# Optimization experiments

Measured on AMD Instinct MI355X. Metric: run time of the kernel, lower is better.

## Reference

```python
import jax, jax.numpy as jnp
import numpy as np

B, OBS, H, A, E = 131072, 194, 64, 5, 3  # batch, obs dim, hidden, max_action_dim, n event types


def setup_inputs() -> dict:
    key = jax.random.key(0)
    ks = jax.random.split(key, 16)
    s = lambda k, shape, std=0.1: (jax.random.normal(k, shape, dtype=jnp.float32) * std)
    return {
        "x": jax.random.normal(ks[0], (B, OBS), dtype=jnp.float32),
        "action": jax.random.randint(ks[1], (B,), 0, A),
        "W1": s(ks[2], (OBS, H)), "b1": jnp.zeros((H,), jnp.float32),
        "W2": s(ks[3], (H, H)),   "b2": jnp.zeros((H,), jnp.float32),
        "Wh": s(ks[4], (E, H, A), 0.01), "bh": jnp.zeros((E, A), jnp.float32),
        "Wc1": s(ks[5], (OBS, H)), "bc1": jnp.zeros((H,), jnp.float32),
        "Wc2": s(ks[6], (H, H)),   "bc2": jnp.zeros((H,), jnp.float32),
        "Wc3": s(ks[7], (H, 1)),   "bc3": jnp.zeros((1,), jnp.float32),
    }


def reference(x, action, W1, b1, W2, b2, Wh, bh, Wc1, bc1, Wc2, bc2, Wc3, bc3):
    # shared trunk
    feat = jnp.tanh(jnp.tanh(x @ W1 + b1) @ W2 + b2)          # [B, H]
    # route each sample to one of E heads via argmax of first 3 obs dims
    ev = jnp.argmax(x[:, :E], axis=1)                          # [B] int
    all_logits = jnp.einsum('bh,eha->bea', feat, Wh) + bh      # [B, E, A]
    logits = jnp.take_along_axis(
        all_logits, jnp.broadcast_to(ev[:, None, None], (x.shape[0], 1, A)), axis=1
    )[:, 0]                                                    # [B, A]
    logp_all = jax.nn.log_softmax(logits, axis=-1)             # [B, A]
    logp = jnp.take_along_axis(logp_all, action[:, None], axis=1)[:, 0]  # [B]
    entropy = -jnp.sum(jnp.exp(logp_all) * logp_all, axis=-1)  # [B]
    # critic
    value = jnp.tanh(jnp.tanh(x @ Wc1 + bc1) @ Wc2 + bc2) @ Wc3 + bc3    # [B, 1]
    return action, logp, entropy, value
```

## Files before the change

### kernel.cpp

```cpp
#include <hip/hip_runtime.h>
#include <hip/hip_bf16.h>

constexpr int Bt  = 131072;
constexpr int OBS = 194;
constexpr int NT  = 256;
constexpr int MT  = 64;
constexpr int RS  = 72;
constexpr int LS  = 18;

constexpr int W1B_S  = 0;
constexpr int WC1B_S = 14336;
constexpr int W2B_S  = 28672;
constexpr int WC2B_S = 36864;
constexpr int WHB_S  = 45056;

typedef short bf8   __attribute__((ext_vector_type(8)));
typedef float f32x4 __attribute__((ext_vector_type(4)));
typedef unsigned int u32;

__device__ __forceinline__ short f2bs(float f) {
    union { __hip_bfloat16 h; short s; } u;
    u.h = __float2bfloat16(f);
    return u.s;
}
__device__ __forceinline__ float bs2f(short s) {
    union { short s; __hip_bfloat16 h; } u;
    u.s = s;
    return __bfloat162float(u.h);
}
__device__ __forceinline__ u32 pk2(float a, float b) {
    union { __hip_bfloat162 h; u32 u; } r;
    r.h = __float22bfloat162_rn(float2{a, b});
    return r.u;
}
__device__ __forceinline__ float fast_tanh(float v) {
    v = fminf(fmaxf(v, -15.f), 15.f);
    float e = __expf(2.f * v);
    return (e - 1.f) * __builtin_amdgcn_rcpf(e + 1.f);
}
__device__ __forceinline__ void dma16(const void* g, void* s) {
    __builtin_amdgcn_global_load_lds(
        (const __attribute__((address_space(1))) u32*)g,
        (__attribute__((address_space(3))) u32*)s, 16, 0, 0);
}

__global__ void __launch_bounds__(256) prep(
    const float* __restrict__ W1, const float* __restrict__ b1,
    const float* __restrict__ W2, const float* __restrict__ Wh,
    const float* __restrict__ Wc1, const float* __restrict__ bc1,
    const float* __restrict__ Wc2, const float* __restrict__ Wc3,
    short* __restrict__ ws)
{
    const int gid = blockIdx.x * 256 + threadIdx.x;
    const int gsz = gridDim.x * 256;

    for (int i = gid; i < 14336; i += gsz) {
        int j = i & 7, l = (i >> 3) & 63, nt = (i >> 9) & 3, kb = i >> 11;
        int k = kb * 32 + ((l >> 4) << 3) + j;
        int n = nt * 16 + (l & 15);
        short v1 = 0, v2 = 0;
        if (k < OBS) {
            v1 = f2bs(W1[k * 64 + n]);
            v2 = f2bs(Wc1[k * 64 + n]);
        } else if (k == OBS) {
            v1 = f2bs(b1[n]);
            v2 = f2bs(bc1[n]);
        }
        ws[W1B_S + i]  = v1;
        ws[WC1B_S + i] = v2;
    }
    for (int i = gid; i < 8192; i += gsz) {
        int j = i & 7, l = (i >> 3) & 63, nt = (i >> 9) & 3, kb = i >> 11;
        int s = kb * 32 + ((l >> 4) << 3) + j;
        int kp = (s & 3) * 16 + (s >> 2);
        int n = nt * 16 + (l & 15);
        ws[W2B_S + i]  = f2bs(W2[kp * 64 + n]);
        ws[WC2B_S + i] = f2bs(Wc2[kp * 64 + n]);
    }
    for (int i = gid; i < 1024; i += gsz) {
        int j = i & 7, l = (i >> 3) & 63, kb = i >> 9;
        int s = kb * 32 + ((l >> 4) << 3) + j;
        int kp = (s & 3) * 16 + (s >> 2);
        int cc = l & 15;
        float v;
        if (cc == 15) v = Wc3[kp];
        else { int e = cc / 5, a = cc - 5 * e; v = Wh[(e * 64 + kp) * 5 + a]; }
        ws[WHB_S + i] = f2bs(v);
    }
}

__global__ void __launch_bounds__(NT, 2) fused_ac(
    const float* __restrict__ x, const int* __restrict__ act_in,
    const float* __restrict__ b2, const float* __restrict__ bc2,
    const float* __restrict__ bh, const float* __restrict__ bc3,
    const short* __restrict__ ws,
    float* __restrict__ out)
{
    __shared__ __align__(16) char smem[57344];

    const int t  = threadIdx.x;
    const int w  = t >> 6;
    const int l  = t & 63;
    const int q  = l >> 4;
    const int c  = l & 15;
    const int gm = blockIdx.x * MT + w * 16 + c;

    {
        const char* g = ((const char*)ws) + (size_t)(w * 14) * 1024 + l * 16;
        char* s = smem + (w * 14) * 1024 + l * 16;
        #pragma unroll
        for (int i = 0; i < 14; ++i)
            dma16(g + i * 1024, s + i * 1024);
    }

    float b2v[4], bc2v[4];
    #pragma unroll
    for (int nt = 0; nt < 4; ++nt) {
        b2v[nt]  = b2[nt * 16 + c];
        bc2v[nt] = bc2[nt * 16 + c];
    }
    float bhv = (c < 15) ? bh[c] : bc3[0];
    int act = 0;
    if (l < 16) act = act_in[gm];

    union AF { u32 u[4]; bf8 v; } af[7];
    int ev = 0;
    {
        const float* xr = x + (size_t)gm * OBS;
        #pragma unroll
        for (int kb = 0; kb < 6; ++kb) {
            const float2* p = reinterpret_cast<const float2*>(xr + kb * 32 + q * 8);
            float2 v0 = p[0], v1 = p[1], v2 = p[2], v3 = p[3];
            if (kb == 0 && q == 0) {
                float best = v0.x;
                if (v0.y > best) { best = v0.y; ev = 1; }
                if (v1.x > best) { ev = 2; }
            }
            af[kb].u[0] = pk2(v0.x, v0.y); af[kb].u[1] = pk2(v1.x, v1.y);
            af[kb].u[2] = pk2(v2.x, v2.y); af[kb].u[3] = pk2(v3.x, v3.y);
        }
        af[6].u[0] = 0; af[6].u[1] = 0; af[6].u[2] = 0; af[6].u[3] = 0;
        if (q == 0) {
            float2 v = *reinterpret_cast<const float2*>(xr + 192);
            af[6].u[0] = pk2(v.x, v.y);
            af[6].u[1] = pk2(1.0f, 0.0f);
        }
    }

    __syncthreads();

    const bf8* fW1L  = reinterpret_cast<const bf8*>(smem);
    const bf8* fWc1L = reinterpret_cast<const bf8*>(smem + 28672);
    f32x4 aa[4], ac[4];
    #pragma unroll
    for (int nt = 0; nt < 4; ++nt) {
        aa[nt] = f32x4{0.f, 0.f, 0.f, 0.f};
        ac[nt] = f32x4{0.f, 0.f, 0.f, 0.f};
    }
    #pragma unroll
    for (int kb = 0; kb < 7; ++kb) {
        bf8 a = af[kb].v;
        #pragma unroll
        for (int nt = 0; nt < 4; ++nt) {
            aa[nt] = __builtin_amdgcn_mfma_f32_16x16x32_bf16(a, fW1L [(kb * 4 + nt) * 64 + l], aa[nt], 0, 0, 0);
            ac[nt] = __builtin_amdgcn_mfma_f32_16x16x32_bf16(a, fWc1L[(kb * 4 + nt) * 64 + l], ac[nt], 0, 0, 0);
        }
    }
    #pragma unroll
    for (int nt = 0; nt < 4; ++nt)
        #pragma unroll
        for (int r = 0; r < 4; ++r) {
            aa[nt][r] = fast_tanh(aa[nt][r]);
            ac[nt][r] = fast_tanh(ac[nt][r]);
        }

    __syncthreads();

    {
        const char* g = ((const char*)ws) + 57344 + (size_t)(w * 9) * 1024 + l * 16;
        char* s = smem + (w * 9) * 1024 + l * 16;
        #pragma unroll
        for (int i = 0; i < 9; ++i)
            if (w * 9 + i < 34)
                dma16(g + i * 1024, s + i * 1024);
    }
    short* ha = reinterpret_cast<short*>(smem + 34816 + w * 2304);
    short* hc = reinterpret_cast<short*>(smem + 44032 + w * 2304);
    #pragma unroll
    for (int r = 0; r < 4; ++r) {
        uint2 pa, pc;
        pa.x = pk2(aa[0][r], aa[1][r]); pa.y = pk2(aa[2][r], aa[3][r]);
        pc.x = pk2(ac[0][r], ac[1][r]); pc.y = pk2(ac[2][r], ac[3][r]);
        *reinterpret_cast<uint2*>(&ha[(q * 4 + r) * RS + 4 * c]) = pa;
        *reinterpret_cast<uint2*>(&hc[(q * 4 + r) * RS + 4 * c]) = pc;
    }

    __syncthreads();

    const bf8* fW2L  = reinterpret_cast<const bf8*>(smem);
    const bf8* fWc2L = reinterpret_cast<const bf8*>(smem + 16384);
    const bf8* fWhL  = reinterpret_cast<const bf8*>(smem + 32768);
    #pragma unroll
    for (int nt = 0; nt < 4; ++nt) {
        aa[nt] = f32x4{b2v[nt], b2v[nt], b2v[nt], b2v[nt]};
        ac[nt] = f32x4{bc2v[nt], bc2v[nt], bc2v[nt], bc2v[nt]};
    }
    #pragma unroll
    for (int kb = 0; kb < 2; ++kb) {
        bf8 xa = *reinterpret_cast<const bf8*>(&ha[c * RS + kb * 32 + q * 8]);
        bf8 xc = *reinterpret_cast<const bf8*>(&hc[c * RS + kb * 32 + q * 8]);
        #pragma unroll
        for (int nt = 0; nt < 4; ++nt) {
            aa[nt] = __builtin_amdgcn_mfma_f32_16x16x32_bf16(xa, fW2L [(kb * 4 + nt) * 64 + l], aa[nt], 0, 0, 0);
            ac[nt] = __builtin_amdgcn_mfma_f32_16x16x32_bf16(xc, fWc2L[(kb * 4 + nt) * 64 + l], ac[nt], 0, 0, 0);
        }
    }
    #pragma unroll
    for (int r = 0; r < 4; ++r) {
        uint2 pa, pc;
        pa.x = pk2(fast_tanh(aa[0][r]), fast_tanh(aa[1][r]));
        pa.y = pk2(fast_tanh(aa[2][r]), fast_tanh(aa[3][r]));
        pc.x = pk2(fast_tanh(ac[0][r]), fast_tanh(ac[1][r]));
        pc.y = pk2(fast_tanh(ac[2][r]), fast_tanh(ac[3][r]));
        *reinterpret_cast<uint2*>(&ha[(q * 4 + r) * RS + 4 * c]) = pa;
        *reinterpret_cast<uint2*>(&hc[(q * 4 + r) * RS + 4 * c]) = pc;
    }

    short* lw = reinterpret_cast<short*>(smem + 53248 + w * 576);
    float* vb = reinterpret_cast<float*>(smem + 55552 + w * 64);
    {
        f32x4 lg = f32x4{bhv, bhv, bhv, bhv};
        f32x4 vv = f32x4{bhv, bhv, bhv, bhv};
        #pragma unroll
        for (int kb = 0; kb < 2; ++kb) {
            bf8 bw = fWhL[kb * 64 + l];
            bf8 fa = *reinterpret_cast<const bf8*>(&ha[c * RS + kb * 32 + q * 8]);
            bf8 fc = *reinterpret_cast<const bf8*>(&hc[c * RS + kb * 32 + q * 8]);
            lg = __builtin_amdgcn_mfma_f32_16x16x32_bf16(fa, bw, lg, 0, 0, 0);
            vv = __builtin_amdgcn_mfma_f32_16x16x32_bf16(fc, bw, vv, 0, 0, 0);
        }
        #pragma unroll
        for (int r = 0; r < 4; ++r)
            lw[(q * 4 + r) * LS + c] = f2bs(lg[r]);
        if (c == 15) {
            #pragma unroll
            for (int r = 0; r < 4; ++r)
                vb[q * 4 + r] = vv[r];
        }
    }

    if (l < 16) {
        float lg[5];
        #pragma unroll
        for (int a = 0; a < 5; ++a)
            lg[a] = bs2f(lw[c * LS + ev * 5 + a]);
        float mx = lg[0];
        #pragma unroll
        for (int a = 1; a < 5; ++a) mx = fmaxf(mx, lg[a]);
        float se = 0.f;
        #pragma unroll
        for (int a = 0; a < 5; ++a) se += __expf(lg[a] - mx);
        float lse = __logf(se) + mx;
        float lsel = lg[0];
        #pragma unroll
        for (int a = 1; a < 5; ++a) lsel = (act == a) ? lg[a] : lsel;
        float ent = 0.f;
        #pragma unroll
        for (int a = 0; a < 5; ++a) { float lp = lg[a] - lse; ent -= __expf(lp) * lp; }

        out[gm]          = (float)act;
        out[Bt + gm]     = lsel - lse;
        out[2 * Bt + gm] = ent;
        out[3 * Bt + gm] = vb[c];
    }
}

extern "C" void kernel_launch(void* const* d_in, const int* in_sizes, int n_in,
                              void* d_out, int out_size, void* d_ws, size_t ws_size,
                              hipStream_t stream) {
    const float* x   = (const float*)d_in[0];
    const int*   act = (const int*)  d_in[1];
    const float* W1  = (const float*)d_in[2];
    const float* b1  = (const float*)d_in[3];
    const float* W2  = (const float*)d_in[4];
    const float* b2  = (const float*)d_in[5];
    const float* Wh  = (const float*)d_in[6];
    const float* bh  = (const float*)d_in[7];
    const float* Wc1 = (const float*)d_in[8];
    const float* bc1 = (const float*)d_in[9];
    const float* Wc2 = (const float*)d_in[10];
    const float* bc2 = (const float*)d_in[11];
    const float* Wc3 = (const float*)d_in[12];
    const float* bc3 = (const float*)d_in[13];
    float* out = (float*)d_out;
    short* ws  = (short*)d_ws;

    hipLaunchKernelGGL(prep, dim3(32), dim3(256), 0, stream,
                       W1, b1, W2, Wh, Wc1, bc1, Wc2, Wc3, ws);
    hipLaunchKernelGGL(fused_ac, dim3(Bt / MT), dim3(NT), 0, stream,
                       x, act, b2, bc2, bh, bc3, ws, out);
}
```

Measured before the change: 186.7 us.

## Keep all weights resident in LDS and loop over row tiles with prefetch

Each block now loads every packed weight matrix into LDS once (about 134 KB), uses 512 threads, and processes 512 rows over four iterations instead of 64 rows per block. The x rows for the next iteration are loaded into registers while the current tile's MFMA chain runs, which overlaps global latency with compute. This cuts the per-block weight reload and the mid-kernel restaging and barriers of the old two-phase LDS reuse. In exchange, occupancy drops to one block per CU because of the LDS footprint, the raw prefetch buffer raises register pressure, and the grid shrinks to 256 blocks.

```diff
diff --git a/kernel.cpp b/kernel.cpp
--- a/kernel.cpp
+++ b/kernel.cpp
@@ -1,18 +1,29 @@
 #include <hip/hip_runtime.h>
 #include <hip/hip_bf16.h>
 
-constexpr int Bt  = 131072;
-constexpr int OBS = 194;
-constexpr int NT  = 256;
-constexpr int MT  = 64;
-constexpr int RS  = 72;
-constexpr int LS  = 18;
+constexpr int Bt    = 131072;
+constexpr int OBS   = 194;
+constexpr int NT    = 512;
+constexpr int RPB   = 512;
+constexpr int ITERS = 4;
+constexpr int RS    = 72;
+constexpr int LS    = 18;
 
 constexpr int W1B_S  = 0;
 constexpr int WC1B_S = 14336;
 constexpr int W2B_S  = 28672;
 constexpr int WC2B_S = 36864;
 constexpr int WHB_S  = 45056;
+
+constexpr int L_W1  = 0;
+constexpr int L_WC1 = 28672;
+constexpr int L_W2  = 57344;
+constexpr int L_WC2 = 73728;
+constexpr int L_WH  = 90112;
+constexpr int L_HA  = 92160;
+constexpr int L_LG  = 129024;
+constexpr int L_VB  = 133632;
+constexpr int L_TOT = 134144;
 
 typedef short bf8   __attribute__((ext_vector_type(8)));
 typedef float f32x4 __attribute__((ext_vector_type(4)));
@@ -96,21 +107,20 @@
     const short* __restrict__ ws,
     float* __restrict__ out)
 {
-    __shared__ __align__(16) char smem[57344];
-
-    const int t  = threadIdx.x;
-    const int w  = t >> 6;
-    const int l  = t & 63;
-    const int q  = l >> 4;
-    const int c  = l & 15;
-    const int gm = blockIdx.x * MT + w * 16 + c;
-
-    {
-        const char* g = ((const char*)ws) + (size_t)(w * 14) * 1024 + l * 16;
-        char* s = smem + (w * 14) * 1024 + l * 16;
-        #pragma unroll
-        for (int i = 0; i < 14; ++i)
-            dma16(g + i * 1024, s + i * 1024);
+    __shared__ __align__(16) char smem[L_TOT];
+
+    const int t    = threadIdx.x;
+    const int w    = t >> 6;
+    const int l    = t & 63;
+    const int q    = l >> 4;
+    const int c    = l & 15;
+    const int base = blockIdx.x * RPB;
+
+    #pragma unroll
+    for (int i = 0; i < 12; ++i) {
+        int idx = i * NT + t;
+        if (idx < 5760)
+            dma16(((const char*)ws) + idx * 16, smem + idx * 16);
     }
 
     float b2v[4], bc2v[4];
@@ -120,158 +130,164 @@
         bc2v[nt] = bc2[nt * 16 + c];
     }
     float bhv = (c < 15) ? bh[c] : bc3[0];
-    int act = 0;
-    if (l < 16) act = act_in[gm];
-
+
+    float2 raw[24]; float2 rt6;
+    auto loadraw = [&](int gm2) {
+        const float* xr = x + (size_t)gm2 * OBS;
+        #pragma unroll
+        for (int kb = 0; kb < 6; ++kb) {
+            const float2* p = reinterpret_cast<const float2*>(xr + kb * 32 + q * 8);
+            raw[kb * 4 + 0] = p[0]; raw[kb * 4 + 1] = p[1];
+            raw[kb * 4 + 2] = p[2]; raw[kb * 4 + 3] = p[3];
+        }
+        rt6 = float2{0.f, 0.f};
+        if (q == 0) rt6 = *reinterpret_cast<const float2*>(xr + 192);
+    };
     union AF { u32 u[4]; bf8 v; } af[7];
     int ev = 0;
-    {
-        const float* xr = x + (size_t)gm * OBS;
+    auto packaf = [&]() {
         #pragma unroll
         for (int kb = 0; kb < 6; ++kb) {
-            const float2* p = reinterpret_cast<const float2*>(xr + kb * 32 + q * 8);
-            float2 v0 = p[0], v1 = p[1], v2 = p[2], v3 = p[3];
-            if (kb == 0 && q == 0) {
-                float best = v0.x;
-                if (v0.y > best) { best = v0.y; ev = 1; }
-                if (v1.x > best) { ev = 2; }
-            }
-            af[kb].u[0] = pk2(v0.x, v0.y); af[kb].u[1] = pk2(v1.x, v1.y);
-            af[kb].u[2] = pk2(v2.x, v2.y); af[kb].u[3] = pk2(v3.x, v3.y);
+            af[kb].u[0] = pk2(raw[kb * 4 + 0].x, raw[kb * 4 + 0].y);
+            af[kb].u[1] = pk2(raw[kb * 4 + 1].x, raw[kb * 4 + 1].y);
+            af[kb].u[2] = pk2(raw[kb * 4 + 2].x, raw[kb * 4 + 2].y);
+            af[kb].u[3] = pk2(raw[kb * 4 + 3].x, raw[kb * 4 + 3].y);
         }
         af[6].u[0] = 0; af[6].u[1] = 0; af[6].u[2] = 0; af[6].u[3] = 0;
         if (q == 0) {
-            float2 v = *reinterpret_cast<const float2*>(xr + 192);
-            af[6].u[0] = pk2(v.x, v.y);
+            af[6].u[0] = pk2(rt6.x, rt6.y);
             af[6].u[1] = pk2(1.0f, 0.0f);
         }
-    }
+        ev = 0;
+        float bbest = raw[0].x;
+        if (raw[0].y > bbest) { bbest = raw[0].y; ev = 1; }
+        if (raw[1].x > bbest) { ev = 2; }
+    };
+
+    loadraw(base + w * 16 + c);
 
     __syncthreads();
 
-    const bf8* fW1L  = reinterpret_cast<const bf8*>(smem);
-    const bf8* fWc1L = reinterpret_cast<const bf8*>(smem + 28672);
-    f32x4 aa[4], ac[4];
-    #pragma unroll
-    for (int nt = 0; nt < 4; ++nt) {
-        aa[nt] = f32x4{0.f, 0.f, 0.f, 0.f};
-        ac[nt] = f32x4{0.f, 0.f, 0.f, 0.f};
-    }
-    #pragma unroll
-    for (int kb = 0; kb < 7; ++kb) {
-        bf8 a = af[kb].v;
+    packaf();
+
+    const bf8* fW1L  = reinterpret_cast<const bf8*>(smem + L_W1);
+    const bf8* fWc1L = reinterpret_cast<const bf8*>(smem + L_WC1);
+    const bf8* fW2L  = reinterpret_cast<const bf8*>(smem + L_W2);
+    const bf8* fWc2L = reinterpret_cast<const bf8*>(smem + L_WC2);
+    const bf8* fWhL  = reinterpret_cast<const bf8*>(smem + L_WH);
+    short* ha = reinterpret_cast<short*>(smem + L_HA + w * 4608);
+    short* hc = ha + 2304 / 2;
+    short* lw = reinterpret_cast<short*>(smem + L_LG + w * 576);
+    float* vb = reinterpret_cast<float*>(smem + L_VB + w * 64);
+
+    #pragma unroll 1
+    for (int i = 0; i < ITERS; ++i) {
+        const int gm = base + i * 128 + w * 16 + c;
+        int act = 0;
+        if (l < 16) act = act_in[gm];
+        const int evc = ev;
+
+        if (i + 1 < ITERS) loadraw(base + (i + 1) * 128 + w * 16 + c);
+
+        f32x4 aa[4], ac[4];
         #pragma unroll
         for (int nt = 0; nt < 4; ++nt) {
-            aa[nt] = __builtin_amdgcn_mfma_f32_16x16x32_bf16(a, fW1L [(kb * 4 + nt) * 64 + l], aa[nt], 0, 0, 0);
-            ac[nt] = __builtin_amdgcn_mfma_f32_16x16x32_bf16(a, fWc1L[(kb * 4 + nt) * 64 + l], ac[nt], 0, 0, 0);
-        }
-    }
-    #pragma unroll
-    for (int nt = 0; nt < 4; ++nt)
+            aa[nt] = f32x4{0.f, 0.f, 0.f, 0.f};
+            ac[nt] = f32x4{0.f, 0.f, 0.f, 0.f};
+        }
+        #pragma unroll
+        for (int kb = 0; kb < 7; ++kb) {
+            bf8 a = af[kb].v;
+            #pragma unroll
+            for (int nt = 0; nt < 4; ++nt) {
+                aa[nt] = __builtin_amdgcn_mfma_f32_16x16x32_bf16(a, fW1L [(kb * 4 + nt) * 64 + l], aa[nt], 0, 0, 0);
+                ac[nt] = __builtin_amdgcn_mfma_f32_16x16x32_bf16(a, fWc1L[(kb * 4 + nt) * 64 + l], ac[nt], 0, 0, 0);
+            }
+        }
         #pragma unroll
         for (int r = 0; r < 4; ++r) {
-            aa[nt][r] = fast_tanh(aa[nt][r]);
-            ac[nt][r] = fast_tanh(ac[nt][r]);
-        }
-
-    __syncthreads();
-
-    {
-        const char* g = ((const char*)ws) + 57344 + (size_t)(w * 9) * 1024 + l * 16;
-        char* s = smem + (w * 9) * 1024 + l * 16;
-        #pragma unroll
-        for (int i = 0; i < 9; ++i)
-            if (w * 9 + i < 34)
-                dma16(g + i * 1024, s + i * 1024);
-    }
-    short* ha = reinterpret_cast<short*>(smem + 34816 + w * 2304);
-    short* hc = reinterpret_cast<short*>(smem + 44032 + w * 2304);
-    #pragma unroll
-    for (int r = 0; r < 4; ++r) {
-        uint2 pa, pc;
-        pa.x = pk2(aa[0][r], aa[1][r]); pa.y = pk2(aa[2][r], aa[3][r]);
-        pc.x = pk2(ac[0][r], ac[1][r]); pc.y = pk2(ac[2][r], ac[3][r]);
-        *reinterpret_cast<uint2*>(&ha[(q * 4 + r) * RS + 4 * c]) = pa;
-        *reinterpret_cast<uint2*>(&hc[(q * 4 + r) * RS + 4 * c]) = pc;
-    }
-
-    __syncthreads();
-
-    const bf8* fW2L  = reinterpret_cast<const bf8*>(smem);
-    const bf8* fWc2L = reinterpret_cast<const bf8*>(smem + 16384);
-    const bf8* fWhL  = reinterpret_cast<const bf8*>(smem + 32768);
-    #pragma unroll
-    for (int nt = 0; nt < 4; ++nt) {
-        aa[nt] = f32x4{b2v[nt], b2v[nt], b2v[nt], b2v[nt]};
-        ac[nt] = f32x4{bc2v[nt], bc2v[nt], bc2v[nt], bc2v[nt]};
-    }
-    #pragma unroll
-    for (int kb = 0; kb < 2; ++kb) {
-        bf8 xa = *reinterpret_cast<const bf8*>(&ha[c * RS + kb * 32 + q * 8]);
-        bf8 xc = *reinterpret_cast<const bf8*>(&hc[c * RS + kb * 32 + q * 8]);
+            uint2 pa, pc;
+            pa.x = pk2(fast_tanh(aa[0][r]), fast_tanh(aa[1][r]));
+            pa.y = pk2(fast_tanh(aa[2][r]), fast_tanh(aa[3][r]));
+            pc.x = pk2(fast_tanh(ac[0][r]), fast_tanh(ac[1][r]));
+            pc.y = pk2(fast_tanh(ac[2][r]), fast_tanh(ac[3][r]));
+            *reinterpret_cast<uint2*>(&ha[(q * 4 + r) * RS + 4 * c]) = pa;
+            *reinterpret_cast<uint2*>(&hc[(q * 4 + r) * RS + 4 * c]) = pc;
+        }
+
         #pragma unroll
         for (int nt = 0; nt < 4; ++nt) {
-            aa[nt] = __builtin_amdgcn_mfma_f32_16x16x32_bf16(xa, fW2L [(kb * 4 + nt) * 64 + l], aa[nt], 0, 0, 0);
-            ac[nt] = __builtin_amdgcn_mfma_f32_16x16x32_bf16(xc, fWc2L[(kb * 4 + nt) * 64 + l], ac[nt], 0, 0, 0);
-        }
-    }
-    #pragma unroll
-    for (int r = 0; r < 4; ++r) {
-        uint2 pa, pc;
-        pa.x = pk2(fast_tanh(aa[0][r]), fast_tanh(aa[1][r]));
-        pa.y = pk2(fast_tanh(aa[2][r]), fast_tanh(aa[3][r]));
-        pc.x = pk2(fast_tanh(ac[0][r]), fast_tanh(ac[1][r]));
-        pc.y = pk2(fast_tanh(ac[2][r]), fast_tanh(ac[3][r]));
-        *reinterpret_cast<uint2*>(&ha[(q * 4 + r) * RS + 4 * c]) = pa;
-        *reinterpret_cast<uint2*>(&hc[(q * 4 + r) * RS + 4 * c]) = pc;
-    }
-
-    short* lw = reinterpret_cast<short*>(smem + 53248 + w * 576);
-    float* vb = reinterpret_cast<float*>(smem + 55552 + w * 64);
-    {
-        f32x4 lg = f32x4{bhv, bhv, bhv, bhv};
-        f32x4 vv = f32x4{bhv, bhv, bhv, bhv};
+            aa[nt] = f32x4{b2v[nt], b2v[nt], b2v[nt], b2v[nt]};
+            ac[nt] = f32x4{bc2v[nt], bc2v[nt], bc2v[nt], bc2v[nt]};
+        }
         #pragma unroll
         for (int kb = 0; kb < 2; ++kb) {
-            bf8 bw = fWhL[kb * 64 + l];
-            bf8 fa = *reinterpret_cast<const bf8*>(&ha[c * RS + kb * 32 + q * 8]);
-            bf8 fc = *reinterpret_cast<const bf8*>(&hc[c * RS + kb * 32 + q * 8]);
-            lg = __builtin_amdgcn_mfma_f32_16x16x32_bf16(fa, bw, lg, 0, 0, 0);
-            vv = __builtin_amdgcn_mfma_f32_16x16x32_bf16(fc, bw, vv, 0, 0, 0);
-        }
-        #pragma unroll
-        for (int r = 0; r < 4; ++r)
-            lw[(q * 4 + r) * LS + c] = f2bs(lg[r]);
-        if (c == 15) {
+            bf8 xa = *reinterpret_cast<const bf8*>(&ha[c * RS + kb * 32 + q * 8]);
+            bf8 xc = *reinterpret_cast<const bf8*>(&hc[c * RS + kb * 32 + q * 8]);
+            #pragma unroll
+            for (int nt = 0; nt < 4; ++nt) {
+                aa[nt] = __builtin_amdgcn_mfma_f32_16x16x32_bf16(xa, fW2L [(kb * 4 + nt) * 64 + l], aa[nt], 0, 0, 0);
+                ac[nt] = __builtin_amdgcn_mfma_f32_16x16x32_bf16(xc, fWc2L[(kb * 4 + nt) * 64 + l], ac[nt], 0, 0, 0);
+            }
+        }
+        #pragma unroll
+        for (int r = 0; r < 4; ++r) {
+            uint2 pa, pc;
+            pa.x = pk2(fast_tanh(aa[0][r]), fast_tanh(aa[1][r]));
+            pa.y = pk2(fast_tanh(aa[2][r]), fast_tanh(aa[3][r]));
+            pc.x = pk2(fast_tanh(ac[0][r]), fast_tanh(ac[1][r]));
+            pc.y = pk2(fast_tanh(ac[2][r]), fast_tanh(ac[3][r]));
+            *reinterpret_cast<uint2*>(&ha[(q * 4 + r) * RS + 4 * c]) = pa;
+            *reinterpret_cast<uint2*>(&hc[(q * 4 + r) * RS + 4 * c]) = pc;
+        }
+
+        {
+            f32x4 lg = f32x4{bhv, bhv, bhv, bhv};
+            f32x4 vv = f32x4{bhv, bhv, bhv, bhv};
+            #pragma unroll
+            for (int kb = 0; kb < 2; ++kb) {
+                bf8 bw = fWhL[kb * 64 + l];
+                bf8 fa = *reinterpret_cast<const bf8*>(&ha[c * RS + kb * 32 + q * 8]);
+                bf8 fc = *reinterpret_cast<const bf8*>(&hc[c * RS + kb * 32 + q * 8]);
+                lg = __builtin_amdgcn_mfma_f32_16x16x32_bf16(fa, bw, lg, 0, 0, 0);
+                vv = __builtin_amdgcn_mfma_f32_16x16x32_bf16(fc, bw, vv, 0, 0, 0);
+            }
             #pragma unroll
             for (int r = 0; r < 4; ++r)
-                vb[q * 4 + r] = vv[r];
-        }
-    }
-
-    if (l < 16) {
-        float lg[5];
-        #pragma unroll
-        for (int a = 0; a < 5; ++a)
-            lg[a] = bs2f(lw[c * LS + ev * 5 + a]);
-        float mx = lg[0];
-        #pragma unroll
-        for (int a = 1; a < 5; ++a) mx = fmaxf(mx, lg[a]);
-        float se = 0.f;
-        #pragma unroll
-        for (int a = 0; a < 5; ++a) se += __expf(lg[a] - mx);
-        float lse = __logf(se) + mx;
-        float lsel = lg[0];
-        #pragma unroll
-        for (int a = 1; a < 5; ++a) lsel = (act == a) ? lg[a] : lsel;
-        float ent = 0.f;
-        #pragma unroll
-        for (int a = 0; a < 5; ++a) { float lp = lg[a] - lse; ent -= __expf(lp) * lp; }
-
-        out[gm]          = (float)act;
-        out[Bt + gm]     = lsel - lse;
-        out[2 * Bt + gm] = ent;
-        out[3 * Bt + gm] = vb[c];
+                lw[(q * 4 + r) * LS + c] = f2bs(lg[r]);
+            if (c == 15) {
+                #pragma unroll
+                for (int r = 0; r < 4; ++r)
+                    vb[q * 4 + r] = vv[r];
+            }
+        }
+
+        if (l < 16) {
+            float lg[5];
+            #pragma unroll
+            for (int a = 0; a < 5; ++a)
+                lg[a] = bs2f(lw[c * LS + evc * 5 + a]);
+            float mx = lg[0];
+            #pragma unroll
+            for (int a = 1; a < 5; ++a) mx = fmaxf(mx, lg[a]);
+            float se = 0.f;
+            #pragma unroll
+            for (int a = 0; a < 5; ++a) se += __expf(lg[a] - mx);
+            float lse = __logf(se) + mx;
+            float lsel = lg[0];
+            #pragma unroll
+            for (int a = 1; a < 5; ++a) lsel = (act == a) ? lg[a] : lsel;
+            float ent = 0.f;
+            #pragma unroll
+            for (int a = 0; a < 5; ++a) { float lp = lg[a] - lse; ent -= __expf(lp) * lp; }
+
+            out[gm]          = (float)act;
+            out[Bt + gm]     = lsel - lse;
+            out[2 * Bt + gm] = ent;
+            out[3 * Bt + gm] = vb[c];
+        }
+
+        if (i + 1 < ITERS) packaf();
     }
 }
 
@@ -297,6 +313,6 @@
 
     hipLaunchKernelGGL(prep, dim3(32), dim3(256), 0, stream,
                        W1, b1, W2, Wh, Wc1, bc1, Wc2, Wc3, ws);
-    hipLaunchKernelGGL(fused_ac, dim3(Bt / MT), dim3(NT), 0, stream,
+    hipLaunchKernelGGL(fused_ac, dim3(Bt / RPB), dim3(NT), 0, stream,
                        x, act, b2, bc2, bh, bc3, ws, out);
 }
```

New measurement: 183.1 us. About the same (-2.0%).
